# Kernel tuning notes

Hardware: AMD Instinct MI355X
Metric: run time of the kernel (lower is better)

Reference implementation:

```python
import jax, jax.numpy as jnp
import numpy as np

N, E, E_LBL = 50000, 800000, 200000
D_IN, H = 128, 128


def setup_inputs() -> dict:
    key = jax.random.key(0)
    ks = jax.random.split(key, 12)
    s = 0.05
    return {
        "x": jax.random.normal(ks[0], (N, D_IN), jnp.float32),
        "edge_index": jax.random.randint(ks[1], (2, E), 0, N, jnp.int64),
        "edge_label_index": jax.random.randint(ks[2], (2, E_LBL), 0, N, jnp.int64),
        "pre_w": jax.random.normal(ks[3], (D_IN, H), jnp.float32) * s,
        "pre_b": jax.random.normal(ks[4], (H,), jnp.float32) * s,
        "Wx": jax.random.normal(ks[5], (3, 2, H, H), jnp.float32) * s,  # gates z,r,h x cheb orders T0,T1
        "bx": jax.random.normal(ks[6], (3, H), jnp.float32) * s,
        "Wh": jax.random.normal(ks[7], (3, 2, H, H), jnp.float32) * s,
        "bh": jax.random.normal(ks[8], (3, H), jnp.float32) * s,
        "post_w": jax.random.normal(ks[9], (H, 2), jnp.float32) * s,
        "post_b": jax.random.normal(ks[10], (2,), jnp.float32) * s,
    }


def reference(x, edge_index, edge_label_index, pre_w, pre_b, Wx, bx, Wh, bh, post_w, post_b):
    n = x.shape[0]
    src, dst = edge_index[0], edge_index[1]

    # Scaled Chebyshev Laplacian (sym norm, lambda_max=2): L_hat = -D^{-1/2} A D^{-1/2}
    # (diagonal of L_hat is exactly 0, so only off-diagonal edge terms remain).
    deg = jax.ops.segment_sum(jnp.ones_like(src, dtype=x.dtype), src, num_segments=n)
    dinv = jnp.where(deg > 0, jax.lax.rsqrt(jnp.maximum(deg, 1.0)), 0.0)
    w = -(dinv[src] * dinv[dst])  # [E]

    def lap(v):  # L_hat @ v : gather src rows, weight, scatter-add at dst
        return jax.ops.segment_sum(w[:, None] * v[src], dst, num_segments=n)

    def cheb(v, Lv, W2, b):  # ChebConv K=2: T0(v)@W0 + T1(v)@W1 + b
        return v @ W2[0] + Lv @ W2[1] + b

    # pre: Linear(input_dim -> hidden)
    Xh = x @ pre_w + pre_b  # [N, H]
    LX = lap(Xh)

    # GConvGRU single step, H0 = 0
    Hc = jnp.zeros_like(Xh)
    LH = lap(Hc)
    Z = jax.nn.sigmoid(cheb(Xh, LX, Wx[0], bx[0]) + cheb(Hc, LH, Wh[0], bh[0]))
    R = jax.nn.sigmoid(cheb(Xh, LX, Wx[1], bx[1]) + cheb(Hc, LH, Wh[1], bh[1]))
    HR = Hc * R
    LHR = lap(HR)
    Ht = jnp.tanh(cheb(Xh, LX, Wx[2], bx[2]) + cheb(HR, LHR, Wh[2], bh[2]))
    Hc = Z * Hc + (1.0 - Z) * Ht

    h = jax.nn.relu(Hc)
    # link decoder: gather endpoints, hadamard, Linear(H->2), sum over logits
    hprod = h[edge_label_index[0]] * h[edge_label_index[1]]  # [E_lbl, H]
    out = hprod @ post_w + post_b  # [E_lbl, 2]
    return jnp.sum(out, axis=-1)  # [E_lbl]
```

## Files before the change

kernel.cpp:

```cpp
#include <hip/hip_runtime.h>
#include <math.h>


#define RND 4096
#define SORT_CAP 1536
#define CAPB 6144

typedef __attribute__((ext_vector_type(4))) float f32x4;
typedef __attribute__((ext_vector_type(8))) short short8;

static __device__ __forceinline__ unsigned short f2b(float f) {
  union { float f; unsigned u; } v; v.f = f;
  unsigned r = (v.u + 0x7fffu + ((v.u >> 16) & 1u)) >> 16;
  return (unsigned short)r;
}
static __device__ __forceinline__ float b2f(unsigned short s) {
  union { unsigned u; float f; } v; v.u = ((unsigned)s) << 16;
  return v.f;
}

__global__ __launch_bounds__(256) void prep_kernel(const float* __restrict__ pre_w, const float* __restrict__ Wx,
                                                   const float* __restrict__ bx, const float* __restrict__ bh,
                                                   const float* __restrict__ post_w, const float* __restrict__ post_b,
                                                   unsigned short* __restrict__ Bt1c, unsigned short* __restrict__ Btc2,
                                                   float* __restrict__ fb2, float* __restrict__ pwsum,
                                                   int* __restrict__ deg, int* __restrict__ binPos, int N) {
  int e = blockIdx.x * 256 + threadIdx.x;
  const int TOT = gridDim.x * 256;
  for (int i = e; i < N; i += TOT) deg[i] = 0;
  if (e < 256) binPos[e] = e * CAPB;
  if (e < 16384) {
    int kc = e >> 12, r = e & 4095, col = r >> 5, kk = r & 31;
    Bt1c[e] = f2b(pre_w[(kc * 32 + kk) * 128 + col]);
  }
  int e2 = e - 16384;
  if (e2 >= 0 && e2 < 65536) {
    int kc = e2 >> 13, r = e2 & 8191, cB = r >> 5, kk = r & 31;
    int k = kc * 32 + kk, half = k >> 7, ki = k & 127;
    int cb = cB >> 7, r7 = cB & 127, nw6 = r7 >> 6, u2 = r7 & 63;
    int g = (u2 >= 32) ? 2 : 0, hcol = cb * 64 + nw6 * 32 + (u2 & 31);
    Btc2[e2] = f2b(Wx[((g * 2 + half) * 128 + ki) * 128 + hcol]);
  }
  int e3 = e - (16384 + 65536);
  if (e3 >= 0 && e3 < 256) {
    int cB = e3;
    int cb = cB >> 7, r7 = cB & 127, nw6 = r7 >> 6, u2 = r7 & 63;
    int g = (u2 >= 32) ? 2 : 0, hcol = cb * 64 + nw6 * 32 + (u2 & 31);
    fb2[cB] = bx[g * 128 + hcol] + bh[g * 128 + hcol];
  }
  int e4 = e - (16384 + 65536 + 256);
  if (e4 >= 0 && e4 < 128) pwsum[e4] = post_w[2 * e4] + post_w[2 * e4 + 1];
  if (e4 == 128) pwsum[128] = post_b[0] + post_b[1];
}

__global__ __launch_bounds__(256) void scatter2_kernel(const int* __restrict__ ei, int* __restrict__ binPos,
                                                       unsigned* __restrict__ bins, int* __restrict__ deg, int E) {
  __shared__ unsigned ent[RND];
  __shared__ unsigned char ebin[RND];
  __shared__ int hist[256], scanbuf[256], lstart[256], lofs[256], gbase[256];
  const int t = threadIdx.x;
  for (long long base = (long long)blockIdx.x * RND; base < E; base += (long long)gridDim.x * RND) {
    int cnt = (int)(((long long)E - base < RND) ? (E - base) : RND);
    if (t < 256) hist[t] = 0;
    __syncthreads();
    unsigned my_e[16]; int my_b[16];
#pragma unroll
    for (int u = 0; u < 16; ++u) {
      int i = u * 256 + t;
      my_b[u] = -1;
      if (i < cnt) {
        int idx = (int)base + i;
        int s = ei[idx], d = ei[E + idx];
        atomicAdd(&deg[s], 1);
        my_b[u] = d >> 8;
        my_e[u] = (unsigned)s | ((unsigned)(d & 255) << 16);
        atomicAdd(&hist[my_b[u]], 1);
      }
    }
    __syncthreads();
    scanbuf[t] = hist[t];
    __syncthreads();
    for (int d = 1; d < 256; d <<= 1) {
      int v = (t >= d) ? scanbuf[t - d] : 0;
      __syncthreads();
      scanbuf[t] += v;
      __syncthreads();
    }
    int excl = scanbuf[t] - hist[t];
    lstart[t] = excl;
    lofs[t] = excl;
    if (hist[t] > 0) gbase[t] = atomicAdd(&binPos[t], hist[t]);
    __syncthreads();
#pragma unroll
    for (int u = 0; u < 16; ++u) {
      if (my_b[u] >= 0) {
        int p = atomicAdd(&lofs[my_b[u]], 1);
        ent[p] = my_e[u];
        ebin[p] = (unsigned char)my_b[u];
      }
    }
    __syncthreads();
    for (int i = t; i < cnt; i += 256) {
      int b = ebin[i];
      int pos = gbase[b] + (i - lstart[b]);
      if (pos < (b + 1) * CAPB) bins[pos] = ent[i];
    }
    __syncthreads();
  }
}

__global__ __launch_bounds__(256) void dinv_kernel(const int* __restrict__ deg, float* __restrict__ dinv, int N) {
  int i = blockIdx.x * 256 + threadIdx.x;
  if (i < N) {
    int d = deg[i];
    dinv[i] = d > 0 ? rsqrtf((float)d) : 0.0f;
  }
}

__global__ __launch_bounds__(256) void gemm1_mfma(const float* __restrict__ x, const unsigned short* __restrict__ Bt1c,
                                                  const float* __restrict__ pre_b, unsigned short* __restrict__ Xq,
                                                  int N) {
  __shared__ unsigned short As[128 * 40];
  __shared__ unsigned short Bs[128 * 40];
  const int t = threadIdx.x;
  const int r0 = blockIdx.x * 128;
  const int w = t >> 6, lane = t & 63;
  const int m = lane & 15, q = lane >> 4;
  const int mw = (w >> 1) * 64, nw = (w & 1) * 64;

  f32x4 acc[4][4];
#pragma unroll
  for (int i = 0; i < 4; ++i)
#pragma unroll
    for (int j = 0; j < 4; ++j) acc[i][j] = {0.f, 0.f, 0.f, 0.f};

  const int arow = t >> 1, aseg = t & 1;
  const bool arow_ok = (r0 + arow) < N;
  const float* asrc0 = &x[(size_t)(r0 + arow) * 128 + aseg * 16];

  float4 cav[4]; short8 cbv0, cbv1;
  {
    if (arow_ok) {
#pragma unroll
      for (int i = 0; i < 4; ++i) cav[i] = *(const float4*)(asrc0 + i * 4);
    } else {
#pragma unroll
      for (int i = 0; i < 4; ++i) cav[i] = make_float4(0.f, 0.f, 0.f, 0.f);
    }
    const char* src = (const char*)Bt1c + t * 32;
    cbv0 = *(const short8*)src;
    cbv1 = *(const short8*)(src + 16);
  }

  for (int kc = 0; kc < 4; ++kc) {
    __syncthreads();
    {
      short8 t0, t1;
#pragma unroll
      for (int i = 0; i < 2; ++i) {
        t0[i * 4 + 0] = (short)f2b(cav[i].x); t0[i * 4 + 1] = (short)f2b(cav[i].y);
        t0[i * 4 + 2] = (short)f2b(cav[i].z); t0[i * 4 + 3] = (short)f2b(cav[i].w);
        t1[i * 4 + 0] = (short)f2b(cav[i + 2].x); t1[i * 4 + 1] = (short)f2b(cav[i + 2].y);
        t1[i * 4 + 2] = (short)f2b(cav[i + 2].z); t1[i * 4 + 3] = (short)f2b(cav[i + 2].w);
      }
      *(short8*)&As[arow * 40 + aseg * 16] = t0;
      *(short8*)&As[arow * 40 + aseg * 16 + 8] = t1;
      int bcol = t >> 1, boff = (t & 1) * 16;
      *(short8*)&Bs[bcol * 40 + boff] = cbv0;
      *(short8*)&Bs[bcol * 40 + boff + 8] = cbv1;
    }
    float4 nav[4]; short8 nbv0, nbv1;
    if (kc < 3) {
      if (arow_ok) {
        const float* src = asrc0 + (kc + 1) * 32;
#pragma unroll
        for (int i = 0; i < 4; ++i) nav[i] = *(const float4*)(src + i * 4);
      } else {
#pragma unroll
        for (int i = 0; i < 4; ++i) nav[i] = make_float4(0.f, 0.f, 0.f, 0.f);
      }
      const char* src = (const char*)Bt1c + (size_t)(kc + 1) * 8192 + t * 32;
      nbv0 = *(const short8*)src;
      nbv1 = *(const short8*)(src + 16);
    }
    __syncthreads();
    short8 af[4], bf[4];
#pragma unroll
    for (int i = 0; i < 4; ++i) af[i] = *(const short8*)&As[(mw + i * 16 + m) * 40 + q * 8];
#pragma unroll
    for (int j = 0; j < 4; ++j) bf[j] = *(const short8*)&Bs[(nw + j * 16 + m) * 40 + q * 8];
#pragma unroll
    for (int i = 0; i < 4; ++i)
#pragma unroll
      for (int j = 0; j < 4; ++j)
        acc[i][j] = __builtin_amdgcn_mfma_f32_16x16x32_bf16(af[i], bf[j], acc[i][j], 0, 0, 0);
    if (kc < 3) {
#pragma unroll
      for (int i = 0; i < 4; ++i) cav[i] = nav[i];
      cbv0 = nbv0; cbv1 = nbv1;
    }
  }

#pragma unroll
  for (int i = 0; i < 4; ++i) {
    int rb = r0 + mw + i * 16 + q * 4;
#pragma unroll
    for (int j = 0; j < 4; ++j) {
      int col = nw + j * 16 + m;
      float bias = pre_b[col];
#pragma unroll
      for (int r = 0; r < 4; ++r) {
        int row = rb + r;
        if (row < N) Xq[(size_t)row * 128 + col] = f2b(acc[i][j][r] + bias);
      }
    }
  }
}

__global__ __launch_bounds__(512) void lap_bin_kernel(const unsigned short* __restrict__ Xq,
                                                      unsigned short* __restrict__ LXc,
                                                      const unsigned* __restrict__ bins,
                                                      const int* __restrict__ binPos,
                                                      const float* __restrict__ dinv, int N) {
  __shared__ unsigned short sortS[SORT_CAP];
  __shared__ float sortW[SORT_CAP];
  __shared__ int hist[64], start[64], scanbuf[64], off[64];
  const int t = threadIdx.x;
  const int bin = blockIdx.x >> 2, qt = blockIdx.x & 3;
  const int lo = bin * CAPB;
  int T = binPos[bin] - lo;
  if (T > CAPB) T = CAPB;
  const unsigned* __restrict__ ebase = &bins[lo];
  if (t < 64) hist[t] = 0;
  __syncthreads();
  for (int i = t; i < T; i += 512) {
    unsigned e = ebase[i];
    int dl = (e >> 16) & 255;
    if ((dl >> 6) == qt) atomicAdd(&hist[dl & 63], 1);
  }
  __syncthreads();
  if (t < 64) scanbuf[t] = hist[t];
  __syncthreads();
  for (int d = 1; d < 64; d <<= 1) {
    int v = (t < 64 && t >= d) ? scanbuf[t - d] : 0;
    __syncthreads();
    if (t < 64) scanbuf[t] += v;
    __syncthreads();
  }
  if (t < 64) { int s0 = scanbuf[t] - hist[t]; start[t] = s0; off[t] = s0; }
  __syncthreads();
  for (int i = t; i < T; i += 512) {
    unsigned e = ebase[i];
    int dl = (e >> 16) & 255;
    if ((dl >> 6) == qt) {
      int s = (int)(e & 0xFFFFu);
      int p = atomicAdd(&off[dl & 63], 1);
      if (p < SORT_CAP) { sortS[p] = (unsigned short)s; sortW[p] = dinv[s]; }
    }
  }
  __syncthreads();
  const int wv = t >> 6, lane = t & 63;
  for (int n = wv; n < 64; n += 8) {
    int node = bin * 256 + qt * 64 + n;
    if (node >= N) break;
    int st = start[n], cnum = hist[n];
    float ax = 0.f, ay = 0.f;
    for (int j = 0; j < cnum; j += 8) {
      unsigned v[8]; float ws[8];
#pragma unroll
      for (int u = 0; u < 8; ++u) {
        int idx = j + u;
        int s = 0; float w = 0.f;
        if (idx < cnum) { s = sortS[st + idx]; w = sortW[st + idx]; }
        ws[u] = w;
        v[u] = *(const unsigned*)((const char*)Xq + (size_t)s * 256 + lane * 4);
      }
#pragma unroll
      for (int u = 0; u < 8; ++u) {
        union { unsigned u32; float f; } fl, fh;
        fl.u32 = v[u] << 16; fh.u32 = v[u] & 0xffff0000u;
        ax += ws[u] * fl.f;
        ay += ws[u] * fh.f;
      }
    }
    float wd = -dinv[node];
    unsigned o = (unsigned)f2b(ax * wd) | ((unsigned)f2b(ay * wd) << 16);
    *(unsigned*)((char*)LXc + (size_t)node * 256 + lane * 4) = o;
  }
}

__global__ __launch_bounds__(256) void gemm2_mfma(const unsigned short* __restrict__ Xq,
                                                  const unsigned short* __restrict__ LXc,
                                                  const unsigned short* __restrict__ Btc2,
                                                  const float* __restrict__ fb2,
                                                  unsigned short* __restrict__ hb, int N) {
  __shared__ unsigned short As[128 * 40];
  __shared__ unsigned short Bs[128 * 40];
  const int t = threadIdx.x;
  const int rb = blockIdx.x >> 1, cb = blockIdx.x & 1;
  const int r0 = rb * 128;
  const int w = t >> 6, lane = t & 63;
  const int m = lane & 15, q = lane >> 4;
  const int mw = (w >> 1) * 64, nw = (w & 1) * 64;

  f32x4 acc[4][4];
#pragma unroll
  for (int i = 0; i < 4; ++i)
#pragma unroll
    for (int j = 0; j < 4; ++j) acc[i][j] = {0.f, 0.f, 0.f, 0.f};

  const int arow = t >> 1;
  const int aoff = (t & 1) * 32;
  const char* aXq = (const char*)Xq + (size_t)(r0 + arow) * 256 + aoff;
  const char* aLX = (const char*)LXc + (size_t)(r0 + arow) * 256 + aoff;
  const char* bsrc0 = (const char*)Btc2 + (size_t)cb * 8192 + t * 32;

  short8 cav0, cav1, cbv0, cbv1;
  cav0 = *(const short8*)aXq;
  cav1 = *(const short8*)(aXq + 16);
  cbv0 = *(const short8*)bsrc0;
  cbv1 = *(const short8*)(bsrc0 + 16);

  for (int kc = 0; kc < 8; ++kc) {
    __syncthreads();
    *(short8*)&As[arow * 40 + (aoff >> 1)] = cav0;
    *(short8*)&As[arow * 40 + (aoff >> 1) + 8] = cav1;
    {
      int bcol = t >> 1, boff = (t & 1) * 16;
      *(short8*)&Bs[bcol * 40 + boff] = cbv0;
      *(short8*)&Bs[bcol * 40 + boff + 8] = cbv1;
    }
    short8 nav0, nav1, nbv0, nbv1;
    if (kc < 7) {
      int kn = kc + 1;
      const char* asrc = (kn < 4) ? (aXq + kn * 64) : (aLX + (kn - 4) * 64);
      nav0 = *(const short8*)asrc;
      nav1 = *(const short8*)(asrc + 16);
      const char* bsrc = bsrc0 + (size_t)kn * 16384;
      nbv0 = *(const short8*)bsrc;
      nbv1 = *(const short8*)(bsrc + 16);
    }
    __syncthreads();
    short8 af[4], bf[4];
#pragma unroll
    for (int i = 0; i < 4; ++i) af[i] = *(const short8*)&As[(mw + i * 16 + m) * 40 + q * 8];
#pragma unroll
    for (int j = 0; j < 4; ++j) bf[j] = *(const short8*)&Bs[(nw + j * 16 + m) * 40 + q * 8];
#pragma unroll
    for (int i = 0; i < 4; ++i)
#pragma unroll
      for (int j = 0; j < 4; ++j)
        acc[i][j] = __builtin_amdgcn_mfma_f32_16x16x32_bf16(af[i], bf[j], acc[i][j], 0, 0, 0);
    if (kc < 7) { cav0 = nav0; cav1 = nav1; cbv0 = nbv0; cbv1 = nbv1; }
  }

#pragma unroll
  for (int i = 0; i < 4; ++i) {
    int rbase = r0 + mw + i * 16 + q * 4;
#pragma unroll
    for (int jz = 0; jz < 2; ++jz) {
      int cBz = cb * 128 + nw + jz * 16 + m;
      int hc = cb * 64 + (nw >> 1) + jz * 16 + m;
      float bz = fb2[cBz], bt = fb2[cBz + 32];
#pragma unroll
      for (int r = 0; r < 4; ++r) {
        int row = rbase + r;
        if (row < N) {
          float zp = acc[i][jz][r] + bz;
          float tp = acc[i][jz + 2][r] + bt;
          float zs = 1.0f / (1.0f + __expf(-zp));
          float th = tanhf(tp);
          hb[(size_t)row * 128 + hc] = f2b(fmaxf((1.0f - zs) * th, 0.0f));
        }
      }
    }
  }
}

__global__ __launch_bounds__(256) void decoder_kernel(const unsigned short* __restrict__ hb,
                                                      const int* __restrict__ eli,
                                                      const float* __restrict__ pwsum, float* __restrict__ out, int M) {
  int t = threadIdx.x;
  int i = blockIdx.x * 16 + (t >> 4);
  int l = t & 15;
  if (i >= M) return;
  int a = eli[i], b = eli[M + i];
  int k = l * 8;
  short8 va = *(const short8*)&hb[(size_t)a * 128 + k];
  short8 vb = *(const short8*)&hb[(size_t)b * 128 + k];
  const float4* pwp = (const float4*)&pwsum[k];
  float4 p0 = pwp[0], p1 = pwp[1];
  float s = 0.0f;
  s += b2f((unsigned short)va[0]) * b2f((unsigned short)vb[0]) * p0.x;
  s += b2f((unsigned short)va[1]) * b2f((unsigned short)vb[1]) * p0.y;
  s += b2f((unsigned short)va[2]) * b2f((unsigned short)vb[2]) * p0.z;
  s += b2f((unsigned short)va[3]) * b2f((unsigned short)vb[3]) * p0.w;
  s += b2f((unsigned short)va[4]) * b2f((unsigned short)vb[4]) * p1.x;
  s += b2f((unsigned short)va[5]) * b2f((unsigned short)vb[5]) * p1.y;
  s += b2f((unsigned short)va[6]) * b2f((unsigned short)vb[6]) * p1.z;
  s += b2f((unsigned short)va[7]) * b2f((unsigned short)vb[7]) * p1.w;
#pragma unroll
  for (int off = 8; off; off >>= 1) s += __shfl_xor(s, off);
  if (l == 0) out[i] = s + pwsum[128];
}

extern "C" void kernel_launch(void* const* d_in, const int* in_sizes, int n_in,
                              void* d_out, int out_size, void* d_ws, size_t ws_size,
                              hipStream_t stream) {
  const float* x      = (const float*)d_in[0];
  const int*   ei     = (const int*)d_in[1];
  const int*   eli    = (const int*)d_in[2];
  const float* pre_w  = (const float*)d_in[3];
  const float* pre_b  = (const float*)d_in[4];
  const float* Wx     = (const float*)d_in[5];
  const float* bx     = (const float*)d_in[6];
  const float* bh     = (const float*)d_in[8];
  const float* post_w = (const float*)d_in[9];
  const float* post_b = (const float*)d_in[10];
  float* out = (float*)d_out;

  const int N = in_sizes[0] / 128;
  const int E = in_sizes[1] / 2;
  const int M = in_sizes[2] / 2;
  const int RB = (N + 127) / 128;
  const int NBIN = (N + 255) / 256;

  char* W = (char*)d_ws;
  size_t o = 0;
  int* deg = (int*)(W + o);       o += (size_t)N * 4;
  int* binPos = (int*)(W + o);    o += 1024;
  float* dinv = (float*)(W + o);  o += (size_t)N * 4;
  o = (o + 255) & ~(size_t)255;
  unsigned* bins = (unsigned*)(W + o); o += (size_t)NBIN * CAPB * 4;
  o = (o + 255) & ~(size_t)255;
  unsigned short* Xq = (unsigned short*)(W + o);  o += (size_t)RB * 128 * 256;
  unsigned short* LXc = (unsigned short*)(W + o); o += (size_t)RB * 128 * 256;
  unsigned short* hb = (unsigned short*)(W + o);  o += (size_t)N * 256;
  unsigned short* Bt1c = (unsigned short*)(W + o); o += 32768;
  unsigned short* Btc2 = (unsigned short*)(W + o); o += 131072;
  float* fb2 = (float*)(W + o);  o += 1024;
  float* pwsum = (float*)(W + o); o += 768;

  prep_kernel<<<322, 256, 0, stream>>>(pre_w, Wx, bx, bh, post_w, post_b, Bt1c, Btc2, fb2, pwsum,
                                       deg, binPos, N);
  gemm1_mfma<<<RB, 256, 0, stream>>>(x, Bt1c, pre_b, Xq, N);
  scatter2_kernel<<<(E + RND - 1) / RND, 256, 0, stream>>>(ei, binPos, bins, deg, E);
  dinv_kernel<<<(N + 255) / 256, 256, 0, stream>>>(deg, dinv, N);
  lap_bin_kernel<<<NBIN * 4, 512, 0, stream>>>(Xq, LXc, bins, binPos, dinv, N);
  gemm2_mfma<<<RB * 2, 256, 0, stream>>>(Xq, LXc, Btc2, fb2, hb, N);
  decoder_kernel<<<(M + 15) / 16, 256, 0, stream>>>(hb, eli, pwsum, out, M);
}
```

Before: 225.0 us.

## Merge GEMM1 and edge binning into one launch, fold dinv into lap kernel

The independent pre-linear GEMM and the edge scatter/binning kernel are merged into a single launch, with block index choosing the role, so both run at once and share a union of shared memory. The separate dinv kernel is removed and the inverse sqrt of degree is computed inside the Laplacian kernel straight from deg. This cuts two launches and lets the GEMM and the scatter overlap. In exchange the shared-memory union takes the larger of the two footprints, which can reduce occupancy for the GEMM blocks, and rsqrt is now recomputed per edge.

```diff
diff --git a/kernel.cpp b/kernel.cpp
--- a/kernel.cpp
+++ b/kernel.cpp
@@ -53,13 +53,130 @@
   if (e4 == 128) pwsum[128] = post_b[0] + post_b[1];
 }
 
-__global__ __launch_bounds__(256) void scatter2_kernel(const int* __restrict__ ei, int* __restrict__ binPos,
-                                                       unsigned* __restrict__ bins, int* __restrict__ deg, int E) {
-  __shared__ unsigned ent[RND];
-  __shared__ unsigned char ebin[RND];
-  __shared__ int hist[256], scanbuf[256], lstart[256], lofs[256], gbase[256];
+union SMemU {
+  struct { unsigned short As[128 * 40]; unsigned short Bs[128 * 40]; } g;
+  struct { unsigned ent[RND]; int hist[256], scanbuf[256], lstart[256],
+           lofs[256], gbase[256]; unsigned char ebin[RND]; } s;
+};
+
+__global__ __launch_bounds__(256) void mega1_kernel(const float* __restrict__ x,
+                                                    const unsigned short* __restrict__ Bt1c,
+                                                    const float* __restrict__ pre_b,
+                                                    unsigned short* __restrict__ Xq,
+                                                    const int* __restrict__ ei, int* __restrict__ binPos,
+                                                    unsigned* __restrict__ bins, int* __restrict__ deg,
+                                                    int N, int E, int RB) {
+  __shared__ SMemU sm;
   const int t = threadIdx.x;
-  for (long long base = (long long)blockIdx.x * RND; base < E; base += (long long)gridDim.x * RND) {
+
+  if ((int)blockIdx.x < RB) {
+    unsigned short* As = sm.g.As;
+    unsigned short* Bs = sm.g.Bs;
+    const int r0 = blockIdx.x * 128;
+    const int w = t >> 6, lane = t & 63;
+    const int m = lane & 15, q = lane >> 4;
+    const int mw = (w >> 1) * 64, nw = (w & 1) * 64;
+
+    f32x4 acc[4][4];
+#pragma unroll
+    for (int i = 0; i < 4; ++i)
+#pragma unroll
+      for (int j = 0; j < 4; ++j) acc[i][j] = {0.f, 0.f, 0.f, 0.f};
+
+    const int arow = t >> 1, aseg = t & 1;
+    const bool arow_ok = (r0 + arow) < N;
+    const float* asrc0 = &x[(size_t)(r0 + arow) * 128 + aseg * 16];
+
+    float4 cav[4]; short8 cbv0, cbv1;
+    {
+      if (arow_ok) {
+#pragma unroll
+        for (int i = 0; i < 4; ++i) cav[i] = *(const float4*)(asrc0 + i * 4);
+      } else {
+#pragma unroll
+        for (int i = 0; i < 4; ++i) cav[i] = make_float4(0.f, 0.f, 0.f, 0.f);
+      }
+      const char* src = (const char*)Bt1c + t * 32;
+      cbv0 = *(const short8*)src;
+      cbv1 = *(const short8*)(src + 16);
+    }
+
+    for (int kc = 0; kc < 4; ++kc) {
+      __syncthreads();
+      {
+        short8 t0, t1;
+#pragma unroll
+        for (int i = 0; i < 2; ++i) {
+          t0[i * 4 + 0] = (short)f2b(cav[i].x); t0[i * 4 + 1] = (short)f2b(cav[i].y);
+          t0[i * 4 + 2] = (short)f2b(cav[i].z); t0[i * 4 + 3] = (short)f2b(cav[i].w);
+          t1[i * 4 + 0] = (short)f2b(cav[i + 2].x); t1[i * 4 + 1] = (short)f2b(cav[i + 2].y);
+          t1[i * 4 + 2] = (short)f2b(cav[i + 2].z); t1[i * 4 + 3] = (short)f2b(cav[i + 2].w);
+        }
+        *(short8*)&As[arow * 40 + aseg * 16] = t0;
+        *(short8*)&As[arow * 40 + aseg * 16 + 8] = t1;
+        int bcol = t >> 1, boff = (t & 1) * 16;
+        *(short8*)&Bs[bcol * 40 + boff] = cbv0;
+        *(short8*)&Bs[bcol * 40 + boff + 8] = cbv1;
+      }
+      float4 nav[4]; short8 nbv0, nbv1;
+      if (kc < 3) {
+        if (arow_ok) {
+          const float* src = asrc0 + (kc + 1) * 32;
+#pragma unroll
+          for (int i = 0; i < 4; ++i) nav[i] = *(const float4*)(src + i * 4);
+        } else {
+#pragma unroll
+          for (int i = 0; i < 4; ++i) nav[i] = make_float4(0.f, 0.f, 0.f, 0.f);
+        }
+        const char* src = (const char*)Bt1c + (size_t)(kc + 1) * 8192 + t * 32;
+        nbv0 = *(const short8*)src;
+        nbv1 = *(const short8*)(src + 16);
+      }
+      __syncthreads();
+      short8 af[4], bf[4];
+#pragma unroll
+      for (int i = 0; i < 4; ++i) af[i] = *(const short8*)&As[(mw + i * 16 + m) * 40 + q * 8];
+#pragma unroll
+      for (int j = 0; j < 4; ++j) bf[j] = *(const short8*)&Bs[(nw + j * 16 + m) * 40 + q * 8];
+#pragma unroll
+      for (int i = 0; i < 4; ++i)
+#pragma unroll
+        for (int j = 0; j < 4; ++j)
+          acc[i][j] = __builtin_amdgcn_mfma_f32_16x16x32_bf16(af[i], bf[j], acc[i][j], 0, 0, 0);
+      if (kc < 3) {
+#pragma unroll
+        for (int i = 0; i < 4; ++i) cav[i] = nav[i];
+        cbv0 = nbv0; cbv1 = nbv1;
+      }
+    }
+
+#pragma unroll
+    for (int i = 0; i < 4; ++i) {
+      int rb2 = r0 + mw + i * 16 + q * 4;
+#pragma unroll
+      for (int j = 0; j < 4; ++j) {
+        int col = nw + j * 16 + m;
+        float bias = pre_b[col];
+#pragma unroll
+        for (int r = 0; r < 4; ++r) {
+          int row = rb2 + r;
+          if (row < N) Xq[(size_t)row * 128 + col] = f2b(acc[i][j][r] + bias);
+        }
+      }
+    }
+    return;
+  }
+
+  unsigned* ent = sm.s.ent;
+  unsigned char* ebin = sm.s.ebin;
+  int* hist = sm.s.hist;
+  int* scanbuf = sm.s.scanbuf;
+  int* lstart = sm.s.lstart;
+  int* lofs = sm.s.lofs;
+  int* gbase = sm.s.gbase;
+  const int sbid = (int)blockIdx.x - RB;
+  const int snum = (int)gridDim.x - RB;
+  for (long long base = (long long)sbid * RND; base < E; base += (long long)snum * RND) {
     int cnt = (int)(((long long)E - base < RND) ? (E - base) : RND);
     if (t < 256) hist[t] = 0;
     __syncthreads();
@@ -109,119 +226,11 @@
   }
 }
 
-__global__ __launch_bounds__(256) void dinv_kernel(const int* __restrict__ deg, float* __restrict__ dinv, int N) {
-  int i = blockIdx.x * 256 + threadIdx.x;
-  if (i < N) {
-    int d = deg[i];
-    dinv[i] = d > 0 ? rsqrtf((float)d) : 0.0f;
-  }
-}
-
-__global__ __launch_bounds__(256) void gemm1_mfma(const float* __restrict__ x, const unsigned short* __restrict__ Bt1c,
-                                                  const float* __restrict__ pre_b, unsigned short* __restrict__ Xq,
-                                                  int N) {
-  __shared__ unsigned short As[128 * 40];
-  __shared__ unsigned short Bs[128 * 40];
-  const int t = threadIdx.x;
-  const int r0 = blockIdx.x * 128;
-  const int w = t >> 6, lane = t & 63;
-  const int m = lane & 15, q = lane >> 4;
-  const int mw = (w >> 1) * 64, nw = (w & 1) * 64;
-
-  f32x4 acc[4][4];
-#pragma unroll
-  for (int i = 0; i < 4; ++i)
-#pragma unroll
-    for (int j = 0; j < 4; ++j) acc[i][j] = {0.f, 0.f, 0.f, 0.f};
-
-  const int arow = t >> 1, aseg = t & 1;
-  const bool arow_ok = (r0 + arow) < N;
-  const float* asrc0 = &x[(size_t)(r0 + arow) * 128 + aseg * 16];
-
-  float4 cav[4]; short8 cbv0, cbv1;
-  {
-    if (arow_ok) {
-#pragma unroll
-      for (int i = 0; i < 4; ++i) cav[i] = *(const float4*)(asrc0 + i * 4);
-    } else {
-#pragma unroll
-      for (int i = 0; i < 4; ++i) cav[i] = make_float4(0.f, 0.f, 0.f, 0.f);
-    }
-    const char* src = (const char*)Bt1c + t * 32;
-    cbv0 = *(const short8*)src;
-    cbv1 = *(const short8*)(src + 16);
-  }
-
-  for (int kc = 0; kc < 4; ++kc) {
-    __syncthreads();
-    {
-      short8 t0, t1;
-#pragma unroll
-      for (int i = 0; i < 2; ++i) {
-        t0[i * 4 + 0] = (short)f2b(cav[i].x); t0[i * 4 + 1] = (short)f2b(cav[i].y);
-        t0[i * 4 + 2] = (short)f2b(cav[i].z); t0[i * 4 + 3] = (short)f2b(cav[i].w);
-        t1[i * 4 + 0] = (short)f2b(cav[i + 2].x); t1[i * 4 + 1] = (short)f2b(cav[i + 2].y);
-        t1[i * 4 + 2] = (short)f2b(cav[i + 2].z); t1[i * 4 + 3] = (short)f2b(cav[i + 2].w);
-      }
-      *(short8*)&As[arow * 40 + aseg * 16] = t0;
-      *(short8*)&As[arow * 40 + aseg * 16 + 8] = t1;
-      int bcol = t >> 1, boff = (t & 1) * 16;
-      *(short8*)&Bs[bcol * 40 + boff] = cbv0;
-      *(short8*)&Bs[bcol * 40 + boff + 8] = cbv1;
-    }
-    float4 nav[4]; short8 nbv0, nbv1;
-    if (kc < 3) {
-      if (arow_ok) {
-        const float* src = asrc0 + (kc + 1) * 32;
-#pragma unroll
-        for (int i = 0; i < 4; ++i) nav[i] = *(const float4*)(src + i * 4);
-      } else {
-#pragma unroll
-        for (int i = 0; i < 4; ++i) nav[i] = make_float4(0.f, 0.f, 0.f, 0.f);
-      }
-      const char* src = (const char*)Bt1c + (size_t)(kc + 1) * 8192 + t * 32;
-      nbv0 = *(const short8*)src;
-      nbv1 = *(const short8*)(src + 16);
-    }
-    __syncthreads();
-    short8 af[4], bf[4];
-#pragma unroll
-    for (int i = 0; i < 4; ++i) af[i] = *(const short8*)&As[(mw + i * 16 + m) * 40 + q * 8];
-#pragma unroll
-    for (int j = 0; j < 4; ++j) bf[j] = *(const short8*)&Bs[(nw + j * 16 + m) * 40 + q * 8];
-#pragma unroll
-    for (int i = 0; i < 4; ++i)
-#pragma unroll
-      for (int j = 0; j < 4; ++j)
-        acc[i][j] = __builtin_amdgcn_mfma_f32_16x16x32_bf16(af[i], bf[j], acc[i][j], 0, 0, 0);
-    if (kc < 3) {
-#pragma unroll
-      for (int i = 0; i < 4; ++i) cav[i] = nav[i];
-      cbv0 = nbv0; cbv1 = nbv1;
-    }
-  }
-
-#pragma unroll
-  for (int i = 0; i < 4; ++i) {
-    int rb = r0 + mw + i * 16 + q * 4;
-#pragma unroll
-    for (int j = 0; j < 4; ++j) {
-      int col = nw + j * 16 + m;
-      float bias = pre_b[col];
-#pragma unroll
-      for (int r = 0; r < 4; ++r) {
-        int row = rb + r;
-        if (row < N) Xq[(size_t)row * 128 + col] = f2b(acc[i][j][r] + bias);
-      }
-    }
-  }
-}
-
 __global__ __launch_bounds__(512) void lap_bin_kernel(const unsigned short* __restrict__ Xq,
                                                       unsigned short* __restrict__ LXc,
                                                       const unsigned* __restrict__ bins,
                                                       const int* __restrict__ binPos,
-                                                      const float* __restrict__ dinv, int N) {
+                                                      const int* __restrict__ deg, int N) {
   __shared__ unsigned short sortS[SORT_CAP];
   __shared__ float sortW[SORT_CAP];
   __shared__ int hist[64], start[64], scanbuf[64], off[64];
@@ -255,7 +264,11 @@
     if ((dl >> 6) == qt) {
       int s = (int)(e & 0xFFFFu);
       int p = atomicAdd(&off[dl & 63], 1);
-      if (p < SORT_CAP) { sortS[p] = (unsigned short)s; sortW[p] = dinv[s]; }
+      if (p < SORT_CAP) {
+        int dg = deg[s];
+        sortS[p] = (unsigned short)s;
+        sortW[p] = dg > 0 ? rsqrtf((float)dg) : 0.0f;
+      }
     }
   }
   __syncthreads();
@@ -283,7 +296,8 @@
         ay += ws[u] * fh.f;
       }
     }
-    float wd = -dinv[node];
+    int dgn = deg[node];
+    float wd = dgn > 0 ? -rsqrtf((float)dgn) : 0.0f;
     unsigned o = (unsigned)f2b(ax * wd) | ((unsigned)f2b(ay * wd) << 16);
     *(unsigned*)((char*)LXc + (size_t)node * 256 + lane * 4) = o;
   }
@@ -424,12 +438,12 @@
   const int M = in_sizes[2] / 2;
   const int RB = (N + 127) / 128;
   const int NBIN = (N + 255) / 256;
+  const int SCAT = (E + RND - 1) / RND;
 
   char* W = (char*)d_ws;
   size_t o = 0;
   int* deg = (int*)(W + o);       o += (size_t)N * 4;
   int* binPos = (int*)(W + o);    o += 1024;
-  float* dinv = (float*)(W + o);  o += (size_t)N * 4;
   o = (o + 255) & ~(size_t)255;
   unsigned* bins = (unsigned*)(W + o); o += (size_t)NBIN * CAPB * 4;
   o = (o + 255) & ~(size_t)255;
@@ -443,10 +457,8 @@
 
   prep_kernel<<<322, 256, 0, stream>>>(pre_w, Wx, bx, bh, post_w, post_b, Bt1c, Btc2, fb2, pwsum,
                                        deg, binPos, N);
-  gemm1_mfma<<<RB, 256, 0, stream>>>(x, Bt1c, pre_b, Xq, N);
-  scatter2_kernel<<<(E + RND - 1) / RND, 256, 0, stream>>>(ei, binPos, bins, deg, E);
-  dinv_kernel<<<(N + 255) / 256, 256, 0, stream>>>(deg, dinv, N);
-  lap_bin_kernel<<<NBIN * 4, 512, 0, stream>>>(Xq, LXc, bins, binPos, dinv, N);
+  mega1_kernel<<<RB + SCAT, 256, 0, stream>>>(x, Bt1c, pre_b, Xq, ei, binPos, bins, deg, N, E, RB);
+  lap_bin_kernel<<<NBIN * 4, 512, 0, stream>>>(Xq, LXc, bins, binPos, deg, N);
   gemm2_mfma<<<RB * 2, 256, 0, stream>>>(Xq, LXc, Btc2, fb2, hb, N);
   decoder_kernel<<<(M + 15) / 16, 256, 0, stream>>>(hb, eli, pwsum, out, M);
 }
```

Result: faster. 213.4 us (-5.1%).
